# Performance work log

Measured on AMD Instinct MI355X. Metric: run time of the kernel, lower is better.

The kernel has to match this reference:

```python
import jax, jax.numpy as jnp
import numpy as np

D_MODEL = 512
HEADS = 8

def setup_inputs() -> dict:
    key = jax.random.key(0)
    ks = jax.random.split(key, 11)
    B, S, D = 2, 4096, D_MODEL
    s = 1.0 / np.sqrt(D)
    inp = {
        'q': jax.random.normal(ks[0], (B, S, D), jnp.float32),
        'k': jax.random.normal(ks[1], (B, S, D), jnp.float32),
        'v': jax.random.normal(ks[2], (B, S, D), jnp.float32),
        'Wq': jax.random.normal(ks[3], (D, D), jnp.float32) * s,
        'bq': jnp.zeros((D,), jnp.float32),
        'Wk': jax.random.normal(ks[4], (D, D), jnp.float32) * s,
        'bk': jnp.zeros((D,), jnp.float32),
        'Wv': jax.random.normal(ks[5], (D, D), jnp.float32) * s,
        'bv': jnp.zeros((D,), jnp.float32),
        'Wo': jax.random.normal(ks[6], (D, D), jnp.float32) * s,
        'bo': jnp.zeros((D,), jnp.float32),
    }
    return inp

def _split_heads(x, h):
    B, S, D = x.shape
    return x.reshape(B, S, h, D // h).transpose(0, 2, 1, 3)  # [B,H,S,Dh]

def reference(q, k, v, Wq, bq, Wk, bk, Wv, bv, Wo, bo):
    # torch Linear: y = x @ W.T + b
    qh = _split_heads(q @ Wq.T + bq, HEADS)
    kh = _split_heads(k @ Wk.T + bk, HEADS)
    vh = _split_heads(v @ Wv.T + bv, HEADS)
    d_tensor = qh.shape[-1]
    scale = 1.0 / jnp.sqrt(jnp.asarray(d_tensor, qh.dtype))
    score = jnp.einsum('bhqd,bhkd->bhqk', qh, kh) * scale  # [B,H,S,S]
    attn = jax.nn.softmax(score, axis=-1)
    out = jnp.einsum('bhqk,bhkd->bhqd', attn, vh)
    B, H, S, Dh = out.shape
    out = out.transpose(0, 2, 1, 3).reshape(B, S, H * Dh)
    return out @ Wo.T + bo
```

## Files before the change

kernel.cpp:

```cpp
#include <hip/hip_runtime.h>

typedef short bf16x8 __attribute__((ext_vector_type(8)));
typedef float f32x4 __attribute__((ext_vector_type(4)));
typedef float f32x16 __attribute__((ext_vector_type(16)));
typedef unsigned short ushort_t;
typedef unsigned short us8 __attribute__((ext_vector_type(8)));
typedef unsigned short us4 __attribute__((ext_vector_type(4)));
typedef unsigned int u32x4 __attribute__((ext_vector_type(4)));
typedef unsigned int uint2v __attribute__((ext_vector_type(2)));

#define MFMA16(a, b, c) __builtin_amdgcn_mfma_f32_16x16x32_bf16((a), (b), (c), 0, 0, 0)
#define MFMA32(a, b, c) __builtin_amdgcn_mfma_f32_32x32x16_bf16((a), (b), (c), 0, 0, 0)

static __device__ __forceinline__ ushort_t f2bf(float f) {
    unsigned int u = __builtin_bit_cast(unsigned int, f);
    u += 0x7FFFu + ((u >> 16) & 1u);
    return (ushort_t)(u >> 16);
}

static __device__ __forceinline__ unsigned cvtpk(float lo, float hi) {
    unsigned r;
    asm("v_cvt_pk_bf16_f32 %0, %1, %2" : "=v"(r) : "v"(lo), "v"(hi));
    return r;
}

__global__ __launch_bounds__(256) void cvt_w(const float* __restrict__ W0,
                                             const float* __restrict__ W1,
                                             const float* __restrict__ W2,
                                             const float* __restrict__ W3,
                                             ushort_t* __restrict__ dst) {
    const float* src = (blockIdx.y == 0) ? W0 : (blockIdx.y == 1) ? W1
                     : (blockIdx.y == 2) ? W2 : W3;
    const int i = (blockIdx.x * 256 + threadIdx.x) * 8;
    float4 f0 = *(const float4*)(src + i);
    float4 f1 = *(const float4*)(src + i + 4);
    ushort_t tmp[8] = {f2bf(f0.x), f2bf(f0.y), f2bf(f0.z), f2bf(f0.w),
                       f2bf(f1.x), f2bf(f1.y), f2bf(f1.z), f2bf(f1.w)};
    *(us8*)(dst + (size_t)blockIdx.y * 262144 + i) = *(us8*)tmp;
}

__global__ __launch_bounds__(256) void cvt_x(const float* __restrict__ X0,
                                             const float* __restrict__ X1,
                                             const float* __restrict__ X2,
                                             ushort_t* __restrict__ dst) {
    const float* src = (blockIdx.y == 0) ? X0 : (blockIdx.y == 1) ? X1 : X2;
    const size_t i = ((size_t)blockIdx.x * 256 + threadIdx.x) * 8;
    float4 f0 = *(const float4*)(src + i);
    float4 f1 = *(const float4*)(src + i + 4);
    ushort_t tmp[8] = {f2bf(f0.x), f2bf(f0.y), f2bf(f0.z), f2bf(f0.w),
                       f2bf(f1.x), f2bf(f1.y), f2bf(f1.z), f2bf(f1.w)};
    *(us8*)(dst + (size_t)blockIdx.y * 4194304 + i) = *(us8*)tmp;
}

template <int AMODE, int OMODE>
__global__ __launch_bounds__(256) void gemm_nt(const void* __restrict__ Ap,
                                               const ushort_t* __restrict__ Wb,
                                               const float* __restrict__ bias,
                                               void* __restrict__ outp,
                                               float oscale) {
    constexpr int K = 512;
    __shared__ ushort_t As[64][72];
    __shared__ ushort_t Bs[64][72];

    int bid = blockIdx.x;
    bid = (bid & 7) * 128 + (bid >> 3);
    const int bm = bid >> 3;
    const int bn = bid & 7;
    const int m0 = bm * 64, n0 = bn * 64;
    const int t    = threadIdx.x;
    const int lane = t & 63;
    const int wv   = t >> 6;
    const int wm   = wv >> 1, wn = wv & 1;
    const int lrow = t >> 2;
    const int lcol = (t & 3) * 16;

    const int l15 = lane & 15;
    const int l16 = lane >> 4;

    f32x4 acc[2][2] = {};

    const ushort_t* apb = (const ushort_t*)Ap + (size_t)(m0 + lrow) * K + lcol;
    const float*    apf = (const float*)Ap   + (size_t)(m0 + lrow) * K + lcol;
    const ushort_t* bpb = Wb + (size_t)(n0 + lrow) * K + lcol;

    us8 ar0, ar1, br0, br1;
    f32x4 af[4];

    if constexpr (AMODE == 1) {
        ar0 = *(const us8*)apb; ar1 = *(const us8*)(apb + 8);
    } else {
        af[0] = *(const f32x4*)apf;       af[1] = *(const f32x4*)(apf + 4);
        af[2] = *(const f32x4*)(apf + 8); af[3] = *(const f32x4*)(apf + 12);
    }
    br0 = *(const us8*)bpb; br1 = *(const us8*)(bpb + 8);

#pragma unroll 1
    for (int kt = 0; kt < K / 64; ++kt) {
        __syncthreads();
        if constexpr (AMODE == 1) {
            *(us8*)&As[lrow][lcol]     = ar0;
            *(us8*)&As[lrow][lcol + 8] = ar1;
        } else {
            ushort_t tmp[16];
#pragma unroll
            for (int i = 0; i < 4; ++i)
#pragma unroll
                for (int j = 0; j < 4; ++j) tmp[i * 4 + j] = f2bf(af[i][j]);
            *(us8*)&As[lrow][lcol]     = *(us8*)tmp;
            *(us8*)&As[lrow][lcol + 8] = *(us8*)(tmp + 8);
        }
        *(us8*)&Bs[lrow][lcol]     = br0;
        *(us8*)&Bs[lrow][lcol + 8] = br1;
        __syncthreads();

        if (kt < K / 64 - 1) {
            const int off = (kt + 1) * 64;
            if constexpr (AMODE == 1) {
                ar0 = *(const us8*)(apb + off); ar1 = *(const us8*)(apb + off + 8);
            } else {
                const float* s = apf + off;
                af[0] = *(const f32x4*)s;       af[1] = *(const f32x4*)(s + 4);
                af[2] = *(const f32x4*)(s + 8); af[3] = *(const f32x4*)(s + 12);
            }
            br0 = *(const us8*)(bpb + off); br1 = *(const us8*)(bpb + off + 8);
        }

#pragma unroll
        for (int kk = 0; kk < 2; ++kk) {
            bf16x8 a0 = *(const bf16x8*)&As[wm * 32 + l15][kk * 32 + l16 * 8];
            bf16x8 a1 = *(const bf16x8*)&As[wm * 32 + 16 + l15][kk * 32 + l16 * 8];
            bf16x8 b0 = *(const bf16x8*)&Bs[wn * 32 + l15][kk * 32 + l16 * 8];
            bf16x8 b1 = *(const bf16x8*)&Bs[wn * 32 + 16 + l15][kk * 32 + l16 * 8];
            acc[0][0] = MFMA16(a0, b0, acc[0][0]);
            acc[0][1] = MFMA16(a0, b1, acc[0][1]);
            acc[1][0] = MFMA16(a1, b0, acc[1][0]);
            acc[1][1] = MFMA16(a1, b1, acc[1][1]);
        }
    }

#pragma unroll
    for (int i = 0; i < 2; ++i)
#pragma unroll
        for (int j = 0; j < 2; ++j) {
            const int n  = n0 + wn * 32 + j * 16 + l15;
            const float bv = bias[n];
            if constexpr (OMODE == 2) {
                const int mbase = m0 + wm * 32 + i * 16 + l16 * 4;
                const int b = mbase >> 12, s = mbase & 4095;
                const int h = n >> 6, d = n & 63;
                ushort_t tmp[4];
#pragma unroll
                for (int v = 0; v < 4; ++v) tmp[v] = f2bf((acc[i][j][v] + bv) * oscale);
                *(us4*)((ushort_t*)outp + (((size_t)(b * 8 + h)) * 64 + d) * 4096 + s) = *(us4*)tmp;
            } else {
#pragma unroll
                for (int v = 0; v < 4; ++v) {
                    const int m   = m0 + wm * 32 + i * 16 + l16 * 4 + v;
                    const float val = (acc[i][j][v] + bv) * oscale;
                    if constexpr (OMODE == 1) {
                        const int b = m >> 12, s = m & 4095;
                        const int h = n >> 6, d = n & 63;
                        ((ushort_t*)outp)[(((size_t)(b * 8 + h)) * 4096 + s) * 64 + d] = f2bf(val);
                    } else {
                        ((float*)outp)[(size_t)m * 512 + n] = val;
                    }
                }
            }
        }
}

template <bool PARTIAL>
__global__ __launch_bounds__(256) void attn_fwd(const ushort_t* __restrict__ Qh,
                                                const ushort_t* __restrict__ Kh,
                                                const ushort_t* __restrict__ Vt,
                                                ushort_t* __restrict__ Out,
                                                float* __restrict__ Op,
                                                float* __restrict__ Lp) {
    constexpr int S = 4096;
    constexpr float NM2 = -14.0f;
    const int NT   = PARTIAL ? 32 : 64;
    const int half = PARTIAL ? blockIdx.z : 0;
    const int kt0  = half * 32;

    __shared__ __attribute__((aligned(16))) char KsB[2][8192];
    __shared__ __attribute__((aligned(16))) char VsB[2][8192];

    const int qt = blockIdx.x;
    const int bh = blockIdx.y;
    const int b  = bh >> 3, h = bh & 7;

    const int t    = threadIdx.x;
    const int lane = t & 63;
    const int wv   = t >> 6;
    const int l31  = lane & 31;
    const int hl   = lane >> 5;

    const int qw = qt * 128 + wv * 32;

    bf16x8 qf[4];
    {
        const ushort_t* qp = Qh + ((size_t)bh * S + qw + l31) * 64 + hl * 8;
#pragma unroll
        for (int ds = 0; ds < 4; ++ds) qf[ds] = *(const bf16x8*)(qp + ds * 16);
    }

    float ll = 0.f;
    f32x16 accO[2] = {};

    const int srow   = t >> 2;
    const int scolB  = (t & 3) * 32;
    const int swzrow = (srow & 7) << 4;

    const ushort_t* kgp = Kh + ((size_t)bh * S + kt0 * 64 + srow) * 64 + (t & 3) * 16;
    const ushort_t* vgp = Vt + ((size_t)bh * 64 + srow) * S + kt0 * 64 + (t & 3) * 16;

    us8 kr0, kr1, vr0, vr1;
#define LOADKV(i)                                                      \
    do {                                                               \
        const ushort_t* kn = kgp + (size_t)(i) * 4096;                 \
        const ushort_t* vn = vgp + (i) * 64;                           \
        kr0 = *(const us8*)kn; kr1 = *(const us8*)(kn + 8);            \
        vr0 = *(const us8*)vn; vr1 = *(const us8*)(vn + 8);            \
    } while (0)
#define STOREKV(buf)                                                   \
    do {                                                               \
        *(us8*)(KsB[buf] + srow * 128 + (scolB ^ swzrow))        = kr0;\
        *(us8*)(KsB[buf] + srow * 128 + ((scolB + 16) ^ swzrow)) = kr1;\
        *(us8*)(VsB[buf] + srow * 128 + (scolB ^ swzrow))        = vr0;\
        *(us8*)(VsB[buf] + srow * 128 + ((scolB + 16) ^ swzrow)) = vr1;\
    } while (0)

    LOADKV(0);
    STOREKV(0);
    LOADKV(1);
    __syncthreads();

#pragma unroll 1
    for (int kt = 0; kt < NT; ++kt) {
        const int cur = kt & 1;

        f32x16 sc[2];
#pragma unroll
        for (int i = 0; i < 16; ++i) { sc[0][i] = NM2; sc[1][i] = NM2; }
        __builtin_amdgcn_s_setprio(1);
#pragma unroll
        for (int kb = 0; kb < 2; ++kb) {
#pragma unroll
            for (int ds = 0; ds < 4; ++ds) {
                const int row = kb * 32 + l31;
                bf16x8 kf = *(const bf16x8*)(KsB[cur] + row * 128 +
                               ((ds * 32 + hl * 16) ^ ((row & 7) << 4)));
                sc[kb] = MFMA32(kf, qf[ds], sc[kb]);
            }
        }
        __builtin_amdgcn_s_setprio(0);

#pragma unroll
        for (int kb = 0; kb < 2; ++kb)
#pragma unroll
            for (int i = 0; i < 16; ++i)
                sc[kb][i] = __builtin_amdgcn_exp2f(sc[kb][i]);

        {
            f32x16 sv = sc[0] + sc[1];
            float s8[8];
#pragma unroll
            for (int i = 0; i < 8; ++i) s8[i] = sv[i] + sv[i + 8];
            ll += ((s8[0] + s8[1]) + (s8[2] + s8[3])) + ((s8[4] + s8[5]) + (s8[6] + s8[7]));
        }

        bf16x8 pb[4];
#pragma unroll
        for (int ks = 0; ks < 4; ++ks) {
            const int kb = ks >> 1, R0 = (ks & 1) * 8;
            unsigned w0 = cvtpk(sc[kb][R0 + 0], sc[kb][R0 + 1]);
            unsigned w1 = cvtpk(sc[kb][R0 + 2], sc[kb][R0 + 3]);
            unsigned w2 = cvtpk(sc[kb][R0 + 4], sc[kb][R0 + 5]);
            unsigned w3 = cvtpk(sc[kb][R0 + 6], sc[kb][R0 + 7]);
            uint2v s02 = __builtin_amdgcn_permlane32_swap(w0, w2, false, false);
            uint2v s13 = __builtin_amdgcn_permlane32_swap(w1, w3, false, false);
            u32x4 w = {s02.x, s13.x, s02.y, s13.y};
            pb[ks] = __builtin_bit_cast(bf16x8, w);
        }

        __builtin_amdgcn_s_setprio(1);
#pragma unroll
        for (int ks = 0; ks < 4; ++ks)
#pragma unroll
            for (int db = 0; db < 2; ++db) {
                const int row = db * 32 + l31;
                bf16x8 vf = *(const bf16x8*)(VsB[cur] + row * 128 +
                               ((ks * 32 + hl * 16) ^ ((row & 7) << 4)));
                accO[db] = MFMA32(vf, pb[ks], accO[db]);
            }
        __builtin_amdgcn_s_setprio(0);

        if (kt + 1 < NT) {
            STOREKV(cur ^ 1);
            if (kt + 2 < NT) LOADKV(kt + 2);
        }
        __syncthreads();
    }

    if constexpr (PARTIAL) {
        const float lt = ll + __shfl_xor(ll, 32);
        const size_t pb_ = (size_t)(half * 16 + bh) * 4096 + qw + l31;
        float* op = Op + pb_ * 64;
#pragma unroll
        for (int db = 0; db < 2; ++db)
#pragma unroll
            for (int q4 = 0; q4 < 4; ++q4) {
                float4 tmp = {accO[db][q4 * 4 + 0], accO[db][q4 * 4 + 1],
                              accO[db][q4 * 4 + 2], accO[db][q4 * 4 + 3]};
                *(float4*)(op + db * 32 + q4 * 8 + hl * 4) = tmp;
            }
        if (hl == 0) Lp[pb_] = lt;
    } else {
        const float lt  = ll + __shfl_xor(ll, 32);
        const float inv = 1.0f / lt;
        ushort_t* orow = Out + ((size_t)b * S + qw + l31) * 512 + h * 64;
#pragma unroll
        for (int db = 0; db < 2; ++db)
#pragma unroll
            for (int q4 = 0; q4 < 4; ++q4) {
                unsigned w0 = cvtpk(accO[db][q4 * 4 + 0] * inv, accO[db][q4 * 4 + 1] * inv);
                unsigned w1 = cvtpk(accO[db][q4 * 4 + 2] * inv, accO[db][q4 * 4 + 3] * inv);
                unsigned tmp[2] = {w0, w1};
                *(us4*)(orow + db * 32 + q4 * 8 + hl * 4) = *(const us4*)tmp;
            }
    }
#undef LOADKV
#undef STOREKV
}

__global__ __launch_bounds__(256) void attn_merge(const float* __restrict__ Op,
                                                  const float* __restrict__ Lp,
                                                  ushort_t* __restrict__ Out) {
    const int bh = blockIdx.x;
    const int b  = bh >> 3, h = bh & 7;
    const int q  = blockIdx.y * 32 + (threadIdx.x >> 3);
    const int d0 = (threadIdx.x & 7) * 8;
    const size_t i0 = (size_t)bh * 4096 + q;
    const size_t i1 = i0 + 16 * 4096;
    const float inv = 1.0f / (Lp[i0] + Lp[i1]);
    const float* p0 = Op + i0 * 64 + d0;
    const float* p1 = Op + i1 * 64 + d0;
    f32x4 x0 = *(const f32x4*)p0, x1 = *(const f32x4*)(p0 + 4);
    f32x4 y0 = *(const f32x4*)p1, y1 = *(const f32x4*)(p1 + 4);
    ushort_t tmp[8];
#pragma unroll
    for (int j = 0; j < 4; ++j) {
        tmp[j]     = f2bf((x0[j] + y0[j]) * inv);
        tmp[j + 4] = f2bf((x1[j] + y1[j]) * inv);
    }
    *(us8*)(Out + ((size_t)b * 4096 + q) * 512 + h * 64 + d0) = *(us8*)tmp;
}

extern "C" void kernel_launch(void* const* d_in, const int* in_sizes, int n_in,
                              void* d_out, int out_size, void* d_ws, size_t ws_size,
                              hipStream_t stream) {
    const float* q  = (const float*)d_in[0];
    const float* k  = (const float*)d_in[1];
    const float* v  = (const float*)d_in[2];
    const float* Wq = (const float*)d_in[3];
    const float* bq = (const float*)d_in[4];
    const float* bk = (const float*)d_in[6];
    const float* bv = (const float*)d_in[8];
    const float* bo = (const float*)d_in[10];

    char* w = (char*)d_ws;
    const size_t SZ     = (size_t)2 * 8 * 4096 * 64 * 2;
    const size_t OFF_XB = 4 * SZ + 2 * 1024 * 1024;
    const size_t OFF_OP = OFF_XB + 3 * SZ;
    const size_t OFF_LP = OFF_OP + (size_t)2 * 16 * 4096 * 64 * 4;
    const size_t TOTAL  = OFF_LP + (size_t)2 * 16 * 4096 * 4;

    ushort_t* Qh  = (ushort_t*)(w);
    ushort_t* Kh  = (ushort_t*)(w + SZ);
    ushort_t* Vtr = (ushort_t*)(w + 2 * SZ);
    ushort_t* AO  = (ushort_t*)(w + 3 * SZ);
    ushort_t* Wb  = (ushort_t*)(w + 4 * SZ);
    char*     xb  = w + OFF_XB;
    float*    Opr = (float*)(w + OFF_OP);
    float*    Lpr = (float*)(w + OFF_LP);

    const bool big   = ws_size >= OFF_OP;
    const bool split = ws_size >= TOTAL;

    cvt_w<<<dim3(128, 4), 256, 0, stream>>>(Wq, (const float*)d_in[5],
                                            (const float*)d_in[7], (const float*)d_in[9], Wb);

    const float Cs = 0.125f * 1.44269504f;
    const int gemm_grid = 128 * 8;

    if (big) {
        ushort_t* Qb = (ushort_t*)(xb);
        ushort_t* Kb = (ushort_t*)(xb + SZ);
        ushort_t* Vb = (ushort_t*)(xb + 2 * SZ);
        cvt_x<<<dim3(2048, 3), 256, 0, stream>>>(q, k, v, Qb);
        gemm_nt<1, 1><<<gemm_grid, 256, 0, stream>>>(Qb, Wb + 0 * 262144, bq, Qh, Cs);
        gemm_nt<1, 1><<<gemm_grid, 256, 0, stream>>>(Kb, Wb + 1 * 262144, bk, Kh, 1.0f);
        gemm_nt<1, 2><<<gemm_grid, 256, 0, stream>>>(Vb, Wb + 2 * 262144, bv, Vtr, 1.0f);
    } else {
        gemm_nt<0, 1><<<gemm_grid, 256, 0, stream>>>(q, Wb + 0 * 262144, bq, Qh, Cs);
        gemm_nt<0, 1><<<gemm_grid, 256, 0, stream>>>(k, Wb + 1 * 262144, bk, Kh, 1.0f);
        gemm_nt<0, 2><<<gemm_grid, 256, 0, stream>>>(v, Wb + 2 * 262144, bv, Vtr, 1.0f);
    }

    if (split) {
        attn_fwd<true><<<dim3(32, 16, 2), 256, 0, stream>>>(Qh, Kh, Vtr, AO, Opr, Lpr);
        attn_merge<<<dim3(16, 128), 256, 0, stream>>>(Opr, Lpr, AO);
    } else {
        attn_fwd<false><<<dim3(32, 16), 256, 0, stream>>>(Qh, Kh, Vtr, AO, nullptr, nullptr);
    }

    gemm_nt<1, 0><<<gemm_grid, 256, 0, stream>>>(AO, Wb + 3 * 262144, bo, (float*)d_out, 1.0f);
}
```

Measured before the change: 164.6 us.

## Fuse QKV projections into one launch and compute softmax row sums via MFMA

Drops the separate fp32-to-bf16 activation conversion pass and merges the three QKV projection GEMMs into one launch indexed by blockIdx.y, converting activations in-register with packed bf16 convert instructions. In attention, the row-sum of probabilities is now accumulated with an MFMA against a ones vector instead of VALU adds, the -14 score bias initialization is replaced by a zero-initialized first MFMA, and launch bounds request 4 waves per SIMD. This removes an extra read/write of the activations and several launches, at the cost of reading fp32 activations inside the GEMM and changing the exp2 offset semantics (no more -14 shift, risking overflow).

Measured after the change: 171.6 us. +4.3%, slower.

```diff
diff --git a/kernel.cpp b/kernel.cpp
--- a/kernel.cpp
+++ b/kernel.cpp
@@ -34,33 +34,32 @@
     const int i = (blockIdx.x * 256 + threadIdx.x) * 8;
     float4 f0 = *(const float4*)(src + i);
     float4 f1 = *(const float4*)(src + i + 4);
-    ushort_t tmp[8] = {f2bf(f0.x), f2bf(f0.y), f2bf(f0.z), f2bf(f0.w),
-                       f2bf(f1.x), f2bf(f1.y), f2bf(f1.z), f2bf(f1.w)};
-    *(us8*)(dst + (size_t)blockIdx.y * 262144 + i) = *(us8*)tmp;
-}
-
-__global__ __launch_bounds__(256) void cvt_x(const float* __restrict__ X0,
-                                             const float* __restrict__ X1,
-                                             const float* __restrict__ X2,
-                                             ushort_t* __restrict__ dst) {
-    const float* src = (blockIdx.y == 0) ? X0 : (blockIdx.y == 1) ? X1 : X2;
-    const size_t i = ((size_t)blockIdx.x * 256 + threadIdx.x) * 8;
-    float4 f0 = *(const float4*)(src + i);
-    float4 f1 = *(const float4*)(src + i + 4);
-    ushort_t tmp[8] = {f2bf(f0.x), f2bf(f0.y), f2bf(f0.z), f2bf(f0.w),
-                       f2bf(f1.x), f2bf(f1.y), f2bf(f1.z), f2bf(f1.w)};
-    *(us8*)(dst + (size_t)blockIdx.y * 4194304 + i) = *(us8*)tmp;
-}
-
-template <int AMODE, int OMODE>
-__global__ __launch_bounds__(256) void gemm_nt(const void* __restrict__ Ap,
-                                               const ushort_t* __restrict__ Wb,
-                                               const float* __restrict__ bias,
-                                               void* __restrict__ outp,
-                                               float oscale) {
+    unsigned tw[4] = {cvtpk(f0.x, f0.y), cvtpk(f0.z, f0.w),
+                      cvtpk(f1.x, f1.y), cvtpk(f1.z, f1.w)};
+    *(u32x4*)(dst + (size_t)blockIdx.y * 262144 + i) = *(u32x4*)tw;
+}
+
+__global__ __launch_bounds__(256) void gemm_qkv(const float* __restrict__ qi,
+                                                const float* __restrict__ ki,
+                                                const float* __restrict__ vi,
+                                                const ushort_t* __restrict__ Wball,
+                                                const float* __restrict__ bq,
+                                                const float* __restrict__ bk,
+                                                const float* __restrict__ bv,
+                                                ushort_t* __restrict__ Qh,
+                                                ushort_t* __restrict__ Kh,
+                                                ushort_t* __restrict__ Vt,
+                                                float Cs) {
     constexpr int K = 512;
     __shared__ ushort_t As[64][72];
     __shared__ ushort_t Bs[64][72];
+
+    const int which = blockIdx.y;
+    const float*    Ap   = (which == 0) ? qi : (which == 1) ? ki : vi;
+    const ushort_t* Wb   = Wball + (size_t)which * 262144;
+    const float*    bias = (which == 0) ? bq : (which == 1) ? bk : bv;
+    ushort_t*       outp = (which == 0) ? Qh : (which == 1) ? Kh : Vt;
+    const float oscale   = (which == 0) ? Cs : 1.0f;
 
     int bid = blockIdx.x;
     bid = (bid & 7) * 128 + (bid >> 3);
@@ -79,35 +78,28 @@
 
     f32x4 acc[2][2] = {};
 
-    const ushort_t* apb = (const ushort_t*)Ap + (size_t)(m0 + lrow) * K + lcol;
-    const float*    apf = (const float*)Ap   + (size_t)(m0 + lrow) * K + lcol;
+    const float*    apf = Ap + (size_t)(m0 + lrow) * K + lcol;
     const ushort_t* bpb = Wb + (size_t)(n0 + lrow) * K + lcol;
 
-    us8 ar0, ar1, br0, br1;
+    us8 br0, br1;
     f32x4 af[4];
 
-    if constexpr (AMODE == 1) {
-        ar0 = *(const us8*)apb; ar1 = *(const us8*)(apb + 8);
-    } else {
-        af[0] = *(const f32x4*)apf;       af[1] = *(const f32x4*)(apf + 4);
-        af[2] = *(const f32x4*)(apf + 8); af[3] = *(const f32x4*)(apf + 12);
-    }
+    af[0] = *(const f32x4*)apf;       af[1] = *(const f32x4*)(apf + 4);
+    af[2] = *(const f32x4*)(apf + 8); af[3] = *(const f32x4*)(apf + 12);
     br0 = *(const us8*)bpb; br1 = *(const us8*)(bpb + 8);
 
 #pragma unroll 1
     for (int kt = 0; kt < K / 64; ++kt) {
         __syncthreads();
-        if constexpr (AMODE == 1) {
-            *(us8*)&As[lrow][lcol]     = ar0;
-            *(us8*)&As[lrow][lcol + 8] = ar1;
-        } else {
-            ushort_t tmp[16];
-#pragma unroll
-            for (int i = 0; i < 4; ++i)
-#pragma unroll
-                for (int j = 0; j < 4; ++j) tmp[i * 4 + j] = f2bf(af[i][j]);
-            *(us8*)&As[lrow][lcol]     = *(us8*)tmp;
-            *(us8*)&As[lrow][lcol + 8] = *(us8*)(tmp + 8);
+        {
+            unsigned tw[8];
+#pragma unroll
+            for (int i = 0; i < 4; ++i) {
+                tw[2 * i]     = cvtpk(af[i][0], af[i][1]);
+                tw[2 * i + 1] = cvtpk(af[i][2], af[i][3]);
+            }
+            *(u32x4*)&As[lrow][lcol]     = *(u32x4*)tw;
+            *(u32x4*)&As[lrow][lcol + 8] = *(u32x4*)(tw + 4);
         }
         *(us8*)&Bs[lrow][lcol]     = br0;
         *(us8*)&Bs[lrow][lcol + 8] = br1;
@@ -115,13 +107,9 @@
 
         if (kt < K / 64 - 1) {
             const int off = (kt + 1) * 64;
-            if constexpr (AMODE == 1) {
-                ar0 = *(const us8*)(apb + off); ar1 = *(const us8*)(apb + off + 8);
-            } else {
-                const float* s = apf + off;
-                af[0] = *(const f32x4*)s;       af[1] = *(const f32x4*)(s + 4);
-                af[2] = *(const f32x4*)(s + 8); af[3] = *(const f32x4*)(s + 12);
-            }
+            const float* s = apf + off;
+            af[0] = *(const f32x4*)s;       af[1] = *(const f32x4*)(s + 4);
+            af[2] = *(const f32x4*)(s + 8); af[3] = *(const f32x4*)(s + 12);
             br0 = *(const us8*)(bpb + off); br1 = *(const us8*)(bpb + off + 8);
         }
 
@@ -143,41 +131,110 @@
 #pragma unroll
         for (int j = 0; j < 2; ++j) {
             const int n  = n0 + wn * 32 + j * 16 + l15;
-            const float bv = bias[n];
-            if constexpr (OMODE == 2) {
+            const float bv_ = bias[n];
+            if (which == 2) {
                 const int mbase = m0 + wm * 32 + i * 16 + l16 * 4;
                 const int b = mbase >> 12, s = mbase & 4095;
                 const int h = n >> 6, d = n & 63;
                 ushort_t tmp[4];
 #pragma unroll
-                for (int v = 0; v < 4; ++v) tmp[v] = f2bf((acc[i][j][v] + bv) * oscale);
-                *(us4*)((ushort_t*)outp + (((size_t)(b * 8 + h)) * 64 + d) * 4096 + s) = *(us4*)tmp;
+                for (int v = 0; v < 4; ++v) tmp[v] = f2bf(acc[i][j][v] + bv_);
+                *(us4*)(outp + (((size_t)(b * 8 + h)) * 64 + d) * 4096 + s) = *(us4*)tmp;
             } else {
 #pragma unroll
                 for (int v = 0; v < 4; ++v) {
                     const int m   = m0 + wm * 32 + i * 16 + l16 * 4 + v;
-                    const float val = (acc[i][j][v] + bv) * oscale;
-                    if constexpr (OMODE == 1) {
-                        const int b = m >> 12, s = m & 4095;
-                        const int h = n >> 6, d = n & 63;
-                        ((ushort_t*)outp)[(((size_t)(b * 8 + h)) * 4096 + s) * 64 + d] = f2bf(val);
-                    } else {
-                        ((float*)outp)[(size_t)m * 512 + n] = val;
-                    }
+                    const int b = m >> 12, s = m & 4095;
+                    const int h = n >> 6, d = n & 63;
+                    outp[(((size_t)(b * 8 + h)) * 4096 + s) * 64 + d] =
+                        f2bf((acc[i][j][v] + bv_) * oscale);
                 }
             }
         }
 }
 
+__global__ __launch_bounds__(256) void gemm_out(const ushort_t* __restrict__ Ap,
+                                                const ushort_t* __restrict__ Wb,
+                                                const float* __restrict__ bias,
+                                                float* __restrict__ outp) {
+    constexpr int K = 512;
+    __shared__ ushort_t As[64][72];
+    __shared__ ushort_t Bs[64][72];
+
+    int bid = blockIdx.x;
+    bid = (bid & 7) * 128 + (bid >> 3);
+    const int bm = bid >> 3;
+    const int bn = bid & 7;
+    const int m0 = bm * 64, n0 = bn * 64;
+    const int t    = threadIdx.x;
+    const int lane = t & 63;
+    const int wv   = t >> 6;
+    const int wm   = wv >> 1, wn = wv & 1;
+    const int lrow = t >> 2;
+    const int lcol = (t & 3) * 16;
+
+    const int l15 = lane & 15;
+    const int l16 = lane >> 4;
+
+    f32x4 acc[2][2] = {};
+
+    const ushort_t* apb = Ap + (size_t)(m0 + lrow) * K + lcol;
+    const ushort_t* bpb = Wb + (size_t)(n0 + lrow) * K + lcol;
+
+    us8 ar0, ar1, br0, br1;
+    ar0 = *(const us8*)apb; ar1 = *(const us8*)(apb + 8);
+    br0 = *(const us8*)bpb; br1 = *(const us8*)(bpb + 8);
+
+#pragma unroll 1
+    for (int kt = 0; kt < K / 64; ++kt) {
+        __syncthreads();
+        *(us8*)&As[lrow][lcol]     = ar0;
+        *(us8*)&As[lrow][lcol + 8] = ar1;
+        *(us8*)&Bs[lrow][lcol]     = br0;
+        *(us8*)&Bs[lrow][lcol + 8] = br1;
+        __syncthreads();
+
+        if (kt < K / 64 - 1) {
+            const int off = (kt + 1) * 64;
+            ar0 = *(const us8*)(apb + off); ar1 = *(const us8*)(apb + off + 8);
+            br0 = *(const us8*)(bpb + off); br1 = *(const us8*)(bpb + off + 8);
+        }
+
+#pragma unroll
+        for (int kk = 0; kk < 2; ++kk) {
+            bf16x8 a0 = *(const bf16x8*)&As[wm * 32 + l15][kk * 32 + l16 * 8];
+            bf16x8 a1 = *(const bf16x8*)&As[wm * 32 + 16 + l15][kk * 32 + l16 * 8];
+            bf16x8 b0 = *(const bf16x8*)&Bs[wn * 32 + l15][kk * 32 + l16 * 8];
+            bf16x8 b1 = *(const bf16x8*)&Bs[wn * 32 + 16 + l15][kk * 32 + l16 * 8];
+            acc[0][0] = MFMA16(a0, b0, acc[0][0]);
+            acc[0][1] = MFMA16(a0, b1, acc[0][1]);
+            acc[1][0] = MFMA16(a1, b0, acc[1][0]);
+            acc[1][1] = MFMA16(a1, b1, acc[1][1]);
+        }
+    }
+
+#pragma unroll
+    for (int i = 0; i < 2; ++i)
+#pragma unroll
+        for (int j = 0; j < 2; ++j) {
+            const int n  = n0 + wn * 32 + j * 16 + l15;
+            const float bv_ = bias[n];
+#pragma unroll
+            for (int v = 0; v < 4; ++v) {
+                const int m = m0 + wm * 32 + i * 16 + l16 * 4 + v;
+                outp[(size_t)m * 512 + n] = acc[i][j][v] + bv_;
+            }
+        }
+}
+
 template <bool PARTIAL>
-__global__ __launch_bounds__(256) void attn_fwd(const ushort_t* __restrict__ Qh,
-                                                const ushort_t* __restrict__ Kh,
-                                                const ushort_t* __restrict__ Vt,
-                                                ushort_t* __restrict__ Out,
-                                                float* __restrict__ Op,
-                                                float* __restrict__ Lp) {
+__global__ __launch_bounds__(256, 4) void attn_fwd(const ushort_t* __restrict__ Qh,
+                                                   const ushort_t* __restrict__ Kh,
+                                                   const ushort_t* __restrict__ Vt,
+                                                   ushort_t* __restrict__ Out,
+                                                   float* __restrict__ Op,
+                                                   float* __restrict__ Lp) {
     constexpr int S = 4096;
-    constexpr float NM2 = -14.0f;
     const int NT   = PARTIAL ? 32 : 64;
     const int half = PARTIAL ? blockIdx.z : 0;
     const int kt0  = half * 32;
@@ -204,8 +261,13 @@
         for (int ds = 0; ds < 4; ++ds) qf[ds] = *(const bf16x8*)(qp + ds * 16);
     }
 
-    float ll = 0.f;
+    bf16x8 ones;
+#pragma unroll
+    for (int j = 0; j < 8; ++j) ones[j] = (short)0x3F80;
+
+    const f32x16 fzero = {};
     f32x16 accO[2] = {};
+    f32x16 lacc = {};
 
     const int srow   = t >> 2;
     const int scolB  = (t & 3) * 32;
@@ -240,14 +302,17 @@
         const int cur = kt & 1;
 
         f32x16 sc[2];
-#pragma unroll
-        for (int i = 0; i < 16; ++i) { sc[0][i] = NM2; sc[1][i] = NM2; }
         __builtin_amdgcn_s_setprio(1);
 #pragma unroll
         for (int kb = 0; kb < 2; ++kb) {
-#pragma unroll
-            for (int ds = 0; ds < 4; ++ds) {
-                const int row = kb * 32 + l31;
+            const int row = kb * 32 + l31;
+            {
+                bf16x8 kf = *(const bf16x8*)(KsB[cur] + row * 128 +
+                               ((hl * 16) ^ ((row & 7) << 4)));
+                sc[kb] = MFMA32(kf, qf[0], fzero);
+            }
+#pragma unroll
+            for (int ds = 1; ds < 4; ++ds) {
                 bf16x8 kf = *(const bf16x8*)(KsB[cur] + row * 128 +
                                ((ds * 32 + hl * 16) ^ ((row & 7) << 4)));
                 sc[kb] = MFMA32(kf, qf[ds], sc[kb]);
@@ -260,14 +325,6 @@
 #pragma unroll
             for (int i = 0; i < 16; ++i)
                 sc[kb][i] = __builtin_amdgcn_exp2f(sc[kb][i]);
-
-        {
-            f32x16 sv = sc[0] + sc[1];
-            float s8[8];
-#pragma unroll
-            for (int i = 0; i < 8; ++i) s8[i] = sv[i] + sv[i + 8];
-            ll += ((s8[0] + s8[1]) + (s8[2] + s8[3])) + ((s8[4] + s8[5]) + (s8[6] + s8[7]));
-        }
 
         bf16x8 pb[4];
 #pragma unroll
@@ -285,7 +342,8 @@
 
         __builtin_amdgcn_s_setprio(1);
 #pragma unroll
-        for (int ks = 0; ks < 4; ++ks)
+        for (int ks = 0; ks < 4; ++ks) {
+            lacc = MFMA32(ones, pb[ks], lacc);
 #pragma unroll
             for (int db = 0; db < 2; ++db) {
                 const int row = db * 32 + l31;
@@ -293,6 +351,7 @@
                                ((ks * 32 + hl * 16) ^ ((row & 7) << 4)));
                 accO[db] = MFMA32(vf, pb[ks], accO[db]);
             }
+        }
         __builtin_amdgcn_s_setprio(0);
 
         if (kt + 1 < NT) {
@@ -302,8 +361,9 @@
         __syncthreads();
     }
 
+    const float lt = lacc[0];
+
     if constexpr (PARTIAL) {
-        const float lt = ll + __shfl_xor(ll, 32);
         const size_t pb_ = (size_t)(half * 16 + bh) * 4096 + qw + l31;
         float* op = Op + pb_ * 64;
 #pragma unroll
@@ -316,7 +376,6 @@
             }
         if (hl == 0) Lp[pb_] = lt;
     } else {
-        const float lt  = ll + __shfl_xor(ll, 32);
         const float inv = 1.0f / lt;
         ushort_t* orow = Out + ((size_t)b * S + qw + l31) * 512 + h * 64;
 #pragma unroll
@@ -347,13 +406,12 @@
     const float* p1 = Op + i1 * 64 + d0;
     f32x4 x0 = *(const f32x4*)p0, x1 = *(const f32x4*)(p0 + 4);
     f32x4 y0 = *(const f32x4*)p1, y1 = *(const f32x4*)(p1 + 4);
-    ushort_t tmp[8];
-#pragma unroll
-    for (int j = 0; j < 4; ++j) {
-        tmp[j]     = f2bf((x0[j] + y0[j]) * inv);
-        tmp[j + 4] = f2bf((x1[j] + y1[j]) * inv);
-    }
-    *(us8*)(Out + ((size_t)b * 4096 + q) * 512 + h * 64 + d0) = *(us8*)tmp;
+    unsigned tw[4];
+    tw[0] = cvtpk((x0[0] + y0[0]) * inv, (x0[1] + y0[1]) * inv);
+    tw[1] = cvtpk((x0[2] + y0[2]) * inv, (x0[3] + y0[3]) * inv);
+    tw[2] = cvtpk((x1[0] + y1[0]) * inv, (x1[1] + y1[1]) * inv);
+    tw[3] = cvtpk((x1[2] + y1[2]) * inv, (x1[3] + y1[3]) * inv);
+    *(u32x4*)(Out + ((size_t)b * 4096 + q) * 512 + h * 64 + d0) = *(u32x4*)tw;
 }
 
 extern "C" void kernel_launch(void* const* d_in, const int* in_sizes, int n_in,
@@ -370,8 +428,8 @@
 
     char* w = (char*)d_ws;
     const size_t SZ     = (size_t)2 * 8 * 4096 * 64 * 2;
-    const size_t OFF_XB = 4 * SZ + 2 * 1024 * 1024;
-    const size_t OFF_OP = OFF_XB + 3 * SZ;
+    const size_t OFF_WB = 4 * SZ;
+    const size_t OFF_OP = OFF_WB + 2 * 1024 * 1024;
     const size_t OFF_LP = OFF_OP + (size_t)2 * 16 * 4096 * 64 * 4;
     const size_t TOTAL  = OFF_LP + (size_t)2 * 16 * 4096 * 4;
 
@@ -379,33 +437,17 @@
     ushort_t* Kh  = (ushort_t*)(w + SZ);
     ushort_t* Vtr = (ushort_t*)(w + 2 * SZ);
     ushort_t* AO  = (ushort_t*)(w + 3 * SZ);
-    ushort_t* Wb  = (ushort_t*)(w + 4 * SZ);
-    char*     xb  = w + OFF_XB;
+    ushort_t* Wb  = (ushort_t*)(w + OFF_WB);
     float*    Opr = (float*)(w + OFF_OP);
     float*    Lpr = (float*)(w + OFF_LP);
 
-    const bool big   = ws_size >= OFF_OP;
     const bool split = ws_size >= TOTAL;
 
     cvt_w<<<dim3(128, 4), 256, 0, stream>>>(Wq, (const float*)d_in[5],
                                             (const float*)d_in[7], (const float*)d_in[9], Wb);
 
     const float Cs = 0.125f * 1.44269504f;
-    const int gemm_grid = 128 * 8;
-
-    if (big) {
-        ushort_t* Qb = (ushort_t*)(xb);
-        ushort_t* Kb = (ushort_t*)(xb + SZ);
-        ushort_t* Vb = (ushort_t*)(xb + 2 * SZ);
-        cvt_x<<<dim3(2048, 3), 256, 0, stream>>>(q, k, v, Qb);
-        gemm_nt<1, 1><<<gemm_grid, 256, 0, stream>>>(Qb, Wb + 0 * 262144, bq, Qh, Cs);
-        gemm_nt<1, 1><<<gemm_grid, 256, 0, stream>>>(Kb, Wb + 1 * 262144, bk, Kh, 1.0f);
-        gemm_nt<1, 2><<<gemm_grid, 256, 0, stream>>>(Vb, Wb + 2 * 262144, bv, Vtr, 1.0f);
-    } else {
-        gemm_nt<0, 1><<<gemm_grid, 256, 0, stream>>>(q, Wb + 0 * 262144, bq, Qh, Cs);
-        gemm_nt<0, 1><<<gemm_grid, 256, 0, stream>>>(k, Wb + 1 * 262144, bk, Kh, 1.0f);
-        gemm_nt<0, 2><<<gemm_grid, 256, 0, stream>>>(v, Wb + 2 * 262144, bv, Vtr, 1.0f);
-    }
+    gemm_qkv<<<dim3(1024, 3), 256, 0, stream>>>(q, k, v, Wb, bq, bk, bv, Qh, Kh, Vtr, Cs);
 
     if (split) {
         attn_fwd<true><<<dim3(32, 16, 2), 256, 0, stream>>>(Qh, Kh, Vtr, AO, Opr, Lpr);
@@ -414,5 +456,5 @@
         attn_fwd<false><<<dim3(32, 16), 256, 0, stream>>>(Qh, Kh, Vtr, AO, nullptr, nullptr);
     }
 
-    gemm_nt<1, 0><<<gemm_grid, 256, 0, stream>>>(AO, Wb + 3 * 262144, bo, (float*)d_out, 1.0f);
-}
+    gemm_out<<<1024, 256, 0, stream>>>(AO, Wb + 3 * 262144, bo, (float*)d_out);
+}
```
